# Optimization experiments

Measured on AMD Instinct MI355X. Metric: run time of the kernel, lower is better.

The kernel has to match this reference:

```python
import jax, jax.numpy as jnp
import numpy as np
from jax import lax


def setup_inputs() -> dict:
    key = jax.random.key(0)
    k1, k2, k3, k4 = jax.random.split(key, 4)
    N, D, B, R, EF = 100000, 256, 64, 32, 32
    storage = jax.random.normal(k1, (N, D), dtype=jnp.float32)
    query = jax.random.normal(k2, (B, D), dtype=jnp.float32)
    graph = jax.random.randint(k3, (N, R), 0, N, dtype=jnp.int32)      # fixed-degree NSW adjacency
    initial = jax.random.randint(k4, (B, EF), 0, N, dtype=jnp.int32)   # random entry points (entry())
    return {"query": query, "storage": storage, "graph": graph,
            "initial": initial, "k": 10, "ef_search": EF}


def reference(query, storage, graph, initial, k, ef_search):
    """Batched greedy best-first NSW search (ef_search fixed expansion steps)."""
    N = storage.shape[0]
    INF = jnp.float32(1e30)

    def sqdist(q, ids):
        diff = storage[ids] - q            # [R, D] gather
        return jnp.sum(diff * diff, axis=-1)

    def search_one(q, init):
        cd = sqdist(q, init)                               # candidate distances [EF]
        visited = jnp.zeros((N,), jnp.bool_).at[init].set(True)
        expanded = jnp.zeros((N,), jnp.bool_)

        def step(state, _):
            cid, cd, visited, expanded = state
            # pick closest unexpanded candidate
            pickd = jnp.where(expanded[cid], INF, cd)
            j = jnp.argmin(pickd)
            u = cid[j]
            expanded = expanded.at[u].set(True)
            # expand neighbors of u
            nbrs = graph[u]                                # [R]
            fresh = ~visited[nbrs]
            nd = jnp.where(fresh, sqdist(q, nbrs), INF)    # skip already-visited
            visited = visited.at[nbrs].set(True)
            # merge candidate pool, keep ef_search best
            all_ids = jnp.concatenate([cid, nbrs])
            all_d = jnp.concatenate([cd, nd])
            negd, idx = lax.top_k(-all_d, ef_search)
            return (all_ids[idx], -negd, visited, expanded), None

        (cid, cd, _, _), _ = lax.scan(step, (init, cd, visited, expanded),
                                      None, length=ef_search)
        negk, idx = lax.top_k(-cd, k)
        return cid[idx], -negk

    topk_ids, topk_dists = jax.vmap(search_one)(query, initial)
    return topk_ids, topk_dists
```

## Files before the change

### kernel.cpp

```cpp
#include <hip/hip_runtime.h>


#define DIMS   256
#define RDEG   32
#define EFPOOL 32
#define KOUT   10
#define NWORDS 3125
#define INF_D  1e30f

typedef unsigned long long u64;

__global__ __launch_bounds__(64, 1) void nsw_wave_kernel(
    const float* __restrict__ query,
    const float* __restrict__ storage,
    const int*   __restrict__ graph,
    const int*   __restrict__ initial,
    float*       __restrict__ out,
    int B)
{
    __shared__ unsigned int visited[NWORDS];
    __shared__ unsigned int expanded[NWORDS];
    __shared__ float4 qsh[DIMS / 4];
    __shared__ float4 rows[RDEG * (DIMS / 4)];
    __shared__ u64    keys[64];
    __shared__ float  sc_d[EFPOOL];
    __shared__ int    sc_id[EFPOOL];

    const int l    = threadIdx.x;
    const int b    = blockIdx.x;
    const int nb   = l & 31;
    const int half = l >> 5;

    for (int i = l; i < NWORDS; i += 64) { visited[i] = 0u; expanded[i] = 0u; }

    qsh[l] = reinterpret_cast<const float4*>(query + (size_t)b * DIMS)[l];

    float pool_d  = INF_D;
    int   pool_id = 0;
    int   u       = 0;
    int   nbid    = initial[b * EFPOOL + nb];

    const int vboff = l << 4;

    for (int s = 0; s <= EFPOOL; ++s) {
        const bool is_init = (s == 0);

        if (!is_init && l == 0) expanded[u >> 5] |= 1u << (u & 31);

        #pragma unroll
        for (int j = 0; j < RDEG; ++j) {
            int gid = __builtin_amdgcn_readlane(nbid, j);
            const char* src = (const char*)(storage + (size_t)gid * DIMS)
                            + (vboff ^ (j << 4));
            __builtin_amdgcn_global_load_lds(
                (const __attribute__((address_space(1))) void*)src,
                (__attribute__((address_space(3))) void*)&rows[j * (DIMS / 4)],
                16, 0, 0);
        }

        unsigned vw = visited[nbid >> 5];
        bool fresh = is_init ? true : !((vw >> (nbid & 31)) & 1u);
        if ((l < 32) && fresh) atomicOr(&visited[nbid >> 5], 1u << (nbid & 31));

        asm volatile("s_waitcnt vmcnt(0)" ::: "memory");
        float a0 = 0.f, a1 = 0.f, a2 = 0.f, a3 = 0.f;
        {
            const float4* rp = rows + nb * (DIMS / 4);
            const float4* qp = qsh + half * 32;
            #pragma unroll
            for (int j = 0; j < 32; ++j) {
                float4 r = rp[(half * 32 + j) ^ nb];
                float4 q = qp[j];
                float d0 = r.x - q.x; a0 = fmaf(d0, d0, a0);
                float d1 = r.y - q.y; a1 = fmaf(d1, d1, a1);
                float d2 = r.z - q.z; a2 = fmaf(d2, d2, a2);
                float d3 = r.w - q.w; a3 = fmaf(d3, d3, a3);
            }
        }
        float part = (a0 + a1) + (a2 + a3);
        float d  = part + __shfl_xor(part, 32, 64);
        float nd = fresh ? d : INF_D;

        {
            float ed  = half ? nd   : pool_d;
            int   eid = half ? nbid : pool_id;
            u64 key = ((u64)__float_as_uint(ed) << 6) | (unsigned)l;
            keys[l] = key;
            int rank = 0;
            #pragma unroll
            for (int j = 0; j < 64; ++j)
                rank += (keys[j] < key) ? 1 : 0;
            if (rank < EFPOOL) { sc_d[rank] = ed; sc_id[rank] = eid; }
            pool_d  = sc_d[nb];
            pool_id = sc_id[nb];
        }

        if (s < EFPOOL) {
            bool unexp = !((expanded[pool_id >> 5] >> (pool_id & 31)) & 1u);
            u64 bm = __ballot(unexp && (l < 32));
            int slot = (bm == 0ull) ? 0 : (__ffsll(bm) - 1);
            u = sc_id[slot];
            nbid = graph[(size_t)u * RDEG + nb];
        }
    }

    if (l < KOUT) {
        out[b * KOUT + l]            = (float)pool_id;
        out[B * KOUT + b * KOUT + l] = pool_d;
    }
}

extern "C" void kernel_launch(void* const* d_in, const int* in_sizes, int n_in,
                              void* d_out, int out_size, void* d_ws, size_t ws_size,
                              hipStream_t stream) {
    const float* query   = (const float*)d_in[0];
    const float* storage = (const float*)d_in[1];
    const int*   graph   = (const int*)d_in[2];
    const int*   initial = (const int*)d_in[3];
    float* out = (float*)d_out;

    const int B = in_sizes[0] / DIMS;

    nsw_wave_kernel<<<B, 64, 0, stream>>>(query, storage, graph, initial, out, B);
}
```

Measured before the change: 242.0 us.

## Split each query's search across four cooperating workgroups via global spin exchange

```diff
diff --git a/kernel.cpp b/kernel.cpp
--- a/kernel.cpp
+++ b/kernel.cpp
@@ -1,89 +1,120 @@
 #include <hip/hip_runtime.h>
 
 
-#define DIMS   256
-#define RDEG   32
-#define EFPOOL 32
-#define KOUT   10
-#define NWORDS 3125
-#define INF_D  1e30f
+#define DIMS    256
+#define RDEG    32
+#define EFPOOL  32
+#define KOUT    10
+#define NWORDS  3125
+#define INF_D   1e30f
+#define NSPLIT  4
+#define ROWS_PB 8
 
 typedef unsigned long long u64;
 
-__global__ __launch_bounds__(64, 1) void nsw_wave_kernel(
+__global__ __launch_bounds__(64, 1) void nsw_coop_kernel(
     const float* __restrict__ query,
     const float* __restrict__ storage,
     const int*   __restrict__ graph,
     const int*   __restrict__ initial,
+    u64*         __restrict__ cand,
     float*       __restrict__ out,
     int B)
 {
     __shared__ unsigned int visited[NWORDS];
     __shared__ unsigned int expanded[NWORDS];
     __shared__ float4 qsh[DIMS / 4];
-    __shared__ float4 rows[RDEG * (DIMS / 4)];
     __shared__ u64    keys[64];
     __shared__ float  sc_d[EFPOOL];
     __shared__ int    sc_id[EFPOOL];
 
-    const int l    = threadIdx.x;
-    const int b    = blockIdx.x;
-    const int nb   = l & 31;
-    const int half = l >> 5;
+    const int l     = threadIdx.x;
+    const int q     = blockIdx.x % B;
+    const int g     = blockIdx.x / B;
+    const int nb    = l & 31;
+    const int half  = l >> 5;
+    const bool dlane = (nb < ROWS_PB);
+    const int slot  = g * ROWS_PB + (nb & 7);
 
     for (int i = l; i < NWORDS; i += 64) { visited[i] = 0u; expanded[i] = 0u; }
 
-    qsh[l] = reinterpret_cast<const float4*>(query + (size_t)b * DIMS)[l];
+    qsh[l] = reinterpret_cast<const float4*>(query + (size_t)q * DIMS)[l];
 
     float pool_d  = INF_D;
     int   pool_id = 0;
     int   u       = 0;
-    int   nbid    = initial[b * EFPOOL + nb];
-
-    const int vboff = l << 4;
 
     for (int s = 0; s <= EFPOOL; ++s) {
-        const bool is_init = (s == 0);
+        const unsigned want = (unsigned)(s + 1);
+        u64* cbuf = cand + ((size_t)(s & 1) * B + q) * EFPOOL;
 
-        if (!is_init && l == 0) expanded[u >> 5] |= 1u << (u & 31);
+        if (s > 0 && l == 0) expanded[u >> 5] |= 1u << (u & 31);
 
-        #pragma unroll
-        for (int j = 0; j < RDEG; ++j) {
-            int gid = __builtin_amdgcn_readlane(nbid, j);
-            const char* src = (const char*)(storage + (size_t)gid * DIMS)
-                            + (vboff ^ (j << 4));
-            __builtin_amdgcn_global_load_lds(
-                (const __attribute__((address_space(1))) void*)src,
-                (__attribute__((address_space(3))) void*)&rows[j * (DIMS / 4)],
-                16, 0, 0);
+        int myid = 0;
+        if (dlane)
+            myid = (s == 0) ? initial[q * EFPOOL + slot]
+                            : graph[(size_t)u * RDEG + slot];
+
+        if (s == 0 && l < 32) {
+            int iid = initial[q * EFPOOL + l];
+            atomicOr(&visited[iid >> 5], 1u << (iid & 31));
         }
 
-        unsigned vw = visited[nbid >> 5];
-        bool fresh = is_init ? true : !((vw >> (nbid & 31)) & 1u);
-        if ((l < 32) && fresh) atomicOr(&visited[nbid >> 5], 1u << (nbid & 31));
+        bool fresh = true;
+        if (s > 0 && dlane)
+            fresh = !((visited[myid >> 5] >> (myid & 31)) & 1u);
 
-        asm volatile("s_waitcnt vmcnt(0)" ::: "memory");
-        float a0 = 0.f, a1 = 0.f, a2 = 0.f, a3 = 0.f;
-        {
-            const float4* rp = rows + nb * (DIMS / 4);
-            const float4* qp = qsh + half * 32;
+        float nd_pub = INF_D;
+        if (dlane) {
+            const float4* sp = reinterpret_cast<const float4*>(
+                storage + (size_t)myid * DIMS) + half * 32;
+            float4 r[32];
+            #pragma unroll
+            for (int j = 0; j < 32; ++j) r[j] = sp[j];
+            float a0 = 0.f, a1 = 0.f, a2 = 0.f, a3 = 0.f;
             #pragma unroll
             for (int j = 0; j < 32; ++j) {
-                float4 r = rp[(half * 32 + j) ^ nb];
-                float4 q = qp[j];
-                float d0 = r.x - q.x; a0 = fmaf(d0, d0, a0);
-                float d1 = r.y - q.y; a1 = fmaf(d1, d1, a1);
-                float d2 = r.z - q.z; a2 = fmaf(d2, d2, a2);
-                float d3 = r.w - q.w; a3 = fmaf(d3, d3, a3);
+                float4 qv = qsh[half * 32 + j];
+                float d0 = r[j].x - qv.x; a0 = fmaf(d0, d0, a0);
+                float d1 = r[j].y - qv.y; a1 = fmaf(d1, d1, a1);
+                float d2 = r[j].z - qv.z; a2 = fmaf(d2, d2, a2);
+                float d3 = r[j].w - qv.w; a3 = fmaf(d3, d3, a3);
             }
+            float part = (a0 + a1) + (a2 + a3);
+            float dmine = part + __shfl_xor(part, 32, 64);
+            nd_pub = fresh ? dmine : INF_D;
         }
-        float part = (a0 + a1) + (a2 + a3);
-        float d  = part + __shfl_xor(part, 32, 64);
-        float nd = fresh ? d : INF_D;
+
+        if (l < ROWS_PB) {
+            u64 w = ((u64)__float_as_uint(nd_pub) << 32)
+                  | ((u64)(unsigned)myid << 7) | (u64)want;
+            __hip_atomic_store(&cbuf[slot], w, __ATOMIC_RELAXED,
+                               __HIP_MEMORY_SCOPE_AGENT);
+        }
+
+        float loc_d = __shfl(nd_pub, nb & 7, 64);
+        int   loc_i = __shfl(myid,  nb & 7, 64);
+
+        float cd = INF_D; int cid = 0;
+        if (l >= 32) {
+            if ((nb >> 3) == g) {
+                cd  = loc_d;
+                cid = loc_i;
+            } else {
+                u64 w;
+                do {
+                    w = __hip_atomic_load(&cbuf[nb], __ATOMIC_RELAXED,
+                                          __HIP_MEMORY_SCOPE_AGENT);
+                } while ((unsigned)(w & 0x7Fu) != want);
+                cd  = __uint_as_float((unsigned)(w >> 32));
+                cid = (int)((w >> 7) & 0x1FFFFu);
+            }
+            atomicOr(&visited[cid >> 5], 1u << (cid & 31));
+        }
 
         {
-            float ed  = half ? nd   : pool_d;
-            int   eid = half ? nbid : pool_id;
+            float ed  = (l >= 32) ? cd  : pool_d;
+            int   eid = (l >= 32) ? cid : pool_id;
             u64 key = ((u64)__float_as_uint(ed) << 6) | (unsigned)l;
             keys[l] = key;
             int rank = 0;
@@ -98,15 +129,14 @@
         if (s < EFPOOL) {
             bool unexp = !((expanded[pool_id >> 5] >> (pool_id & 31)) & 1u);
             u64 bm = __ballot(unexp && (l < 32));
-            int slot = (bm == 0ull) ? 0 : (__ffsll(bm) - 1);
-            u = sc_id[slot];
-            nbid = graph[(size_t)u * RDEG + nb];
+            int sl = (bm == 0ull) ? 0 : (__ffsll(bm) - 1);
+            u = sc_id[sl];
         }
     }
 
-    if (l < KOUT) {
-        out[b * KOUT + l]            = (float)pool_id;
-        out[B * KOUT + b * KOUT + l] = pool_d;
+    if (g == 0 && l < KOUT) {
+        out[q * KOUT + l]            = (float)pool_id;
+        out[B * KOUT + q * KOUT + l] = pool_d;
     }
 }
 
@@ -121,5 +151,9 @@
 
     const int B = in_sizes[0] / DIMS;
 
-    nsw_wave_kernel<<<B, 64, 0, stream>>>(query, storage, graph, initial, out, B);
+    const size_t cand_bytes = (size_t)2 * B * EFPOOL * sizeof(u64);
+    hipMemsetAsync(d_ws, 0, cand_bytes, stream);
+
+    nsw_coop_kernel<<<B * NSPLIT, 64, 0, stream>>>(
+        query, storage, graph, initial, (u64*)d_ws, out, B);
 }
```

After: 259.6 us. 7.3% more time.
